# Kernel optimization log

Hardware: AMD Instinct MI355X
Metric: run time of the kernel (lower is better)

## Reference

```python
import jax, jax.numpy as jnp
import numpy as np

N, E = 20000, 200000
DIM, EDGE_DIM, HID = 128, 64, 256


def _linear_init(key, fan_in, fan_out):
    # torch nn.Linear default: U(-1/sqrt(fan_in), 1/sqrt(fan_in)) for W and b
    kw, kb = jax.random.split(key)
    bound = 1.0 / np.sqrt(fan_in)
    W = jax.random.uniform(kw, (fan_in, fan_out), minval=-bound, maxval=bound, dtype=jnp.float32)
    b = jax.random.uniform(kb, (fan_out,), minval=-bound, maxval=bound, dtype=jnp.float32)
    return W, b


def setup_inputs() -> dict:
    key = jax.random.key(0)
    ks = jax.random.split(key, 8)
    H = jax.random.normal(ks[0], (N, DIM), dtype=jnp.float32)
    src = jax.random.randint(ks[1], (E,), 0, N, dtype=jnp.int32)
    dst = jax.random.randint(ks[2], (E,), 0, N, dtype=jnp.int32)
    edge_index = jnp.stack([src, dst], axis=0)
    edge_attr = jax.random.normal(ks[3], (E, EDGE_DIM), dtype=jnp.float32)
    msg_W1, msg_b1 = _linear_init(ks[4], DIM + EDGE_DIM, HID)
    msg_W2, msg_b2 = _linear_init(ks[5], HID, DIM)
    self_W1, self_b1 = _linear_init(ks[6], DIM, HID)
    self_W2, self_b2 = _linear_init(ks[7], HID, DIM)
    eps = jnp.zeros((1,), dtype=jnp.float32)
    return dict(H=H, edge_index=edge_index, edge_attr=edge_attr, eps=eps,
                msg_W1=msg_W1, msg_b1=msg_b1, msg_W2=msg_W2, msg_b2=msg_b2,
                self_W1=self_W1, self_b1=self_b1, self_W2=self_W2, self_b2=self_b2)


def _mlp(x, W1, b1, W2, b2):
    h = jax.nn.relu(x @ W1 + b1)
    return h @ W2 + b2


def reference(H, edge_index, edge_attr, eps,
              msg_W1, msg_b1, msg_W2, msg_b2,
              self_W1, self_b1, self_W2, self_b2):
    src, dst = edge_index[0], edge_index[1]
    # gather source node features, concat edge features -> per-edge message MLP
    msg_in = jnp.concatenate([H[src], edge_attr], axis=-1)  # [E, dim+edge_dim]
    msg = _mlp(msg_in, msg_W1, msg_b1, msg_W2, msg_b2)       # [E, dim]
    # scatter-add messages to destination nodes
    agg = jax.ops.segment_sum(msg, dst, num_segments=H.shape[0])  # [N, dim]
    return _mlp((1.0 + eps) * H + agg, self_W1, self_b1, self_W2, self_b2)
```

## Files before the change

kernel.cpp:

```cpp
#include <hip/hip_runtime.h>

typedef float  f32x4  __attribute__((ext_vector_type(4)));
typedef short  bf16x8 __attribute__((ext_vector_type(8)));
typedef unsigned short u16;

#define NN   20000
#define NE   200000
#define DIM  128
#define EDIM 64
#define HID  256
#define KIN  192

__device__ __forceinline__ u16 f2b(float f) {
  unsigned u = __float_as_uint(f);
  u += 0x7FFFu + ((u >> 16) & 1u);
  return (u16)(u >> 16);
}
__device__ __forceinline__ float b2f(u16 v) {
  return __uint_as_float(((unsigned)v) << 16);
}

__global__ void prep_kernel(const float* __restrict__ mW1, const float* __restrict__ mW2,
                            const float* __restrict__ sW1, const float* __restrict__ sW2,
                            u16* __restrict__ W1T, u16* __restrict__ W2T,
                            u16* __restrict__ S1T, u16* __restrict__ S2T) {
  int t  = blockIdx.x * blockDim.x + threadIdx.x;
  int nt = gridDim.x * blockDim.x;
  for (int i = t; i < KIN * HID; i += nt) { int k = i / HID, n = i % HID; W1T[n * KIN + k] = f2b(mW1[i]); }
  for (int i = t; i < HID * DIM; i += nt) { int k = i / DIM, n = i % DIM; W2T[n * HID + k] = f2b(mW2[i]); }
  for (int i = t; i < DIM * HID; i += nt) { int k = i / HID, n = i % HID; S1T[n * DIM + k] = f2b(sW1[i]); }
  for (int i = t; i < HID * DIM; i += nt) { int k = i / DIM, n = i % DIM; S2T[n * HID + k] = f2b(sW2[i]); }
}

__global__ void hist_kernel(const int* __restrict__ EI, int* __restrict__ cnt) {
  int i = blockIdx.x * 256 + threadIdx.x;
  if (i < NE) atomicAdd(&cnt[EI[NE + i]], 1);
}

__global__ __launch_bounds__(1024) void scan_kernel(const int* __restrict__ cnt,
                                                    int* __restrict__ start,
                                                    int* __restrict__ cursor) {
  __shared__ int ls[1024];
  const int t = threadIdx.x;
  const int base = t * 20;
  int v[20]; int s = 0;
  #pragma unroll
  for (int j = 0; j < 20; ++j) {
    int idx = base + j;
    int c = (idx < NN) ? cnt[idx] : 0;
    v[j] = s; s += c;
  }
  ls[t] = s;
  __syncthreads();
  for (int off = 1; off < 1024; off <<= 1) {
    int x = (t >= off) ? ls[t - off] : 0;
    __syncthreads();
    ls[t] += x;
    __syncthreads();
  }
  int boff = (t > 0) ? ls[t - 1] : 0;
  #pragma unroll
  for (int j = 0; j < 20; ++j) {
    int idx = base + j;
    if (idx < NN) { int val = boff + v[j]; start[idx] = val; cursor[idx] = val; }
  }
  if (t == 0) start[NN] = NE;
}

__global__ __launch_bounds__(256, 4) void edge_kernel(
    const float* __restrict__ H, const int* __restrict__ EI,
    const float* __restrict__ EA,
    const u16* __restrict__ W1T, const float* __restrict__ b1p,
    const u16* __restrict__ W2T, const float* __restrict__ b2p,
    int* __restrict__ cursor, u16* __restrict__ msg) {
  __shared__ int src_s[64];
  __shared__ int pos_s[64];
  __shared__ u16 smem[64 * HID];

  const int tid = threadIdx.x;
  const int e0  = blockIdx.x * 64;
  if (tid < 64) {
    int e = e0 + tid;
    src_s[tid] = EI[e];
    pos_s[tid] = atomicAdd(&cursor[EI[NE + e]], 1);
  }
  __syncthreads();

  #pragma unroll
  for (int i = 0; i < 8; ++i) {
    int idx = tid + i * 256;
    int row = idx >> 5, c4 = idx & 31;
    const float4 v = reinterpret_cast<const float4*>(H + (size_t)src_s[row] * DIM)[c4];
    int by = (c4 * 8) ^ ((row & 7) << 4);
    ushort4 o; o.x = f2b(v.x); o.y = f2b(v.y); o.z = f2b(v.z); o.w = f2b(v.w);
    *reinterpret_cast<ushort4*>(&smem[row * KIN + (by >> 1)]) = o;
  }
  #pragma unroll
  for (int i = 0; i < 4; ++i) {
    int idx = tid + i * 256;
    int row = idx >> 4, c4 = idx & 15;
    const float4 v = reinterpret_cast<const float4*>(EA + (size_t)(e0 + row) * EDIM)[c4];
    int by = (256 + c4 * 8) ^ ((row & 7) << 4);
    ushort4 o; o.x = f2b(v.x); o.y = f2b(v.y); o.z = f2b(v.z); o.w = f2b(v.w);
    *reinterpret_cast<ushort4*>(&smem[row * KIN + (by >> 1)]) = o;
  }
  __syncthreads();

  const int wv = tid >> 6, lane = tid & 63;
  const int lr = lane & 15, lg = lane >> 4;
  const f32x4 zero = {0.f, 0.f, 0.f, 0.f};

  const int n0 = wv * 64;
  f32x4 acc[4][4];
  #pragma unroll
  for (int m = 0; m < 4; ++m)
    #pragma unroll
    for (int n = 0; n < 4; ++n) acc[m][n] = zero;
  float bias1[4];
  #pragma unroll
  for (int n = 0; n < 4; ++n) bias1[n] = b1p[n0 + n * 16 + lr];

  #pragma unroll
  for (int kt = 0; kt < 6; ++kt) {
    bf16x8 af[4], bf[4];
    #pragma unroll
    for (int m = 0; m < 4; ++m) {
      int row = m * 16 + lr;
      int by  = (kt * 64 + lg * 16) ^ ((row & 7) << 4);
      af[m] = *reinterpret_cast<const bf16x8*>(&smem[row * KIN + (by >> 1)]);
    }
    #pragma unroll
    for (int n = 0; n < 4; ++n) {
      int nabs = n0 + n * 16 + lr;
      bf[n] = *reinterpret_cast<const bf16x8*>(&W1T[nabs * KIN + kt * 32 + lg * 8]);
    }
    #pragma unroll
    for (int m = 0; m < 4; ++m)
      #pragma unroll
      for (int n = 0; n < 4; ++n)
        acc[m][n] = __builtin_amdgcn_mfma_f32_16x16x32_bf16(af[m], bf[n], acc[m][n], 0, 0, 0);
  }
  __syncthreads();

  #pragma unroll
  for (int m = 0; m < 4; ++m)
    #pragma unroll
    for (int n = 0; n < 4; ++n)
      #pragma unroll
      for (int r = 0; r < 4; ++r) {
        int row = m * 16 + lg * 4 + r;
        int col = n0 + n * 16 + lr;
        float v = acc[m][n][r] + bias1[n];
        v = fmaxf(v, 0.0f);
        int by = (col * 2) ^ ((row & 7) << 4);
        smem[row * HID + (by >> 1)] = f2b(v);
      }
  __syncthreads();

  const int n0b = wv * 32;
  f32x4 acc2[4][2];
  #pragma unroll
  for (int m = 0; m < 4; ++m) { acc2[m][0] = zero; acc2[m][1] = zero; }
  float bias2[2];
  #pragma unroll
  for (int n = 0; n < 2; ++n) bias2[n] = b2p[n0b + n * 16 + lr];

  #pragma unroll
  for (int kt = 0; kt < 8; ++kt) {
    bf16x8 af[4], bf[2];
    #pragma unroll
    for (int m = 0; m < 4; ++m) {
      int row = m * 16 + lr;
      int by  = (kt * 64 + lg * 16) ^ ((row & 7) << 4);
      af[m] = *reinterpret_cast<const bf16x8*>(&smem[row * HID + (by >> 1)]);
    }
    #pragma unroll
    for (int n = 0; n < 2; ++n) {
      int nabs = n0b + n * 16 + lr;
      bf[n] = *reinterpret_cast<const bf16x8*>(&W2T[nabs * HID + kt * 32 + lg * 8]);
    }
    #pragma unroll
    for (int m = 0; m < 4; ++m)
      #pragma unroll
      for (int n = 0; n < 2; ++n)
        acc2[m][n] = __builtin_amdgcn_mfma_f32_16x16x32_bf16(af[m], bf[n], acc2[m][n], 0, 0, 0);
  }

  #pragma unroll
  for (int m = 0; m < 4; ++m)
    #pragma unroll
    for (int n = 0; n < 2; ++n) {
      int col = n0b + n * 16 + lr;
      float bb = bias2[n];
      #pragma unroll
      for (int r = 0; r < 4; ++r) {
        int row = m * 16 + lg * 4 + r;
        msg[(size_t)pos_s[row] * DIM + col] = f2b(acc2[m][n][r] + bb);
      }
    }
}

__global__ __launch_bounds__(256, 6) void node_kernel(
    const float* __restrict__ H, const u16* __restrict__ msg,
    const int* __restrict__ start_g, const float* __restrict__ epsp,
    const u16* __restrict__ S1T, const float* __restrict__ b1p,
    const u16* __restrict__ S2T, const float* __restrict__ b2p,
    float* __restrict__ out) {
  __shared__ int start_s[33];
  __shared__ u16 smem[32 * HID];
  const int tid = threadIdx.x;
  const int r0  = blockIdx.x * 32;
  const float sc = 1.0f + epsp[0];

  if (tid < 33) start_s[tid] = start_g[r0 + tid];
  __syncthreads();

  {
    const int node = tid >> 3;
    const int c0   = (tid & 7) * 16;
    float a[16];
    #pragma unroll
    for (int j = 0; j < 16; ++j) a[j] = 0.f;
    const int s0 = start_s[node], s1 = start_s[node + 1];
    for (int i = s0; i < s1; ++i) {
      const u16* rp = msg + (size_t)i * DIM + c0;
      bf16x8 lo = *reinterpret_cast<const bf16x8*>(rp);
      bf16x8 hi = *reinterpret_cast<const bf16x8*>(rp + 8);
      #pragma unroll
      for (int j = 0; j < 8; ++j) {
        a[j]     += b2f((u16)lo[j]);
        a[8 + j] += b2f((u16)hi[j]);
      }
    }
    const int gr = r0 + node;
    const float4* hp = reinterpret_cast<const float4*>(H + (size_t)gr * DIM + c0);
    #pragma unroll
    for (int q = 0; q < 4; ++q) {
      float4 h = hp[q];
      ushort4 o;
      o.x = f2b(sc * h.x + a[q * 4 + 0]);
      o.y = f2b(sc * h.y + a[q * 4 + 1]);
      o.z = f2b(sc * h.z + a[q * 4 + 2]);
      o.w = f2b(sc * h.w + a[q * 4 + 3]);
      int col = c0 + q * 4;
      int by = (col * 2) ^ ((node & 7) << 4);
      *reinterpret_cast<ushort4*>(&smem[node * DIM + (by >> 1)]) = o;
    }
  }
  __syncthreads();

  const int wv = tid >> 6, lane = tid & 63;
  const int lr = lane & 15, lg = lane >> 4;
  const f32x4 zero = {0.f, 0.f, 0.f, 0.f};

  const int n0 = wv * 64;
  f32x4 acc[2][4];
  #pragma unroll
  for (int m = 0; m < 2; ++m)
    #pragma unroll
    for (int n = 0; n < 4; ++n) acc[m][n] = zero;
  float bias1[4];
  #pragma unroll
  for (int n = 0; n < 4; ++n) bias1[n] = b1p[n0 + n * 16 + lr];

  #pragma unroll
  for (int kt = 0; kt < 4; ++kt) {
    bf16x8 af[2], bf[4];
    #pragma unroll
    for (int m = 0; m < 2; ++m) {
      int row = m * 16 + lr;
      int by  = (kt * 64 + lg * 16) ^ ((row & 7) << 4);
      af[m] = *reinterpret_cast<const bf16x8*>(&smem[row * DIM + (by >> 1)]);
    }
    #pragma unroll
    for (int n = 0; n < 4; ++n) {
      int nabs = n0 + n * 16 + lr;
      bf[n] = *reinterpret_cast<const bf16x8*>(&S1T[nabs * DIM + kt * 32 + lg * 8]);
    }
    #pragma unroll
    for (int m = 0; m < 2; ++m)
      #pragma unroll
      for (int n = 0; n < 4; ++n)
        acc[m][n] = __builtin_amdgcn_mfma_f32_16x16x32_bf16(af[m], bf[n], acc[m][n], 0, 0, 0);
  }
  __syncthreads();

  #pragma unroll
  for (int m = 0; m < 2; ++m)
    #pragma unroll
    for (int n = 0; n < 4; ++n)
      #pragma unroll
      for (int r = 0; r < 4; ++r) {
        int row = m * 16 + lg * 4 + r;
        int col = n0 + n * 16 + lr;
        float v = acc[m][n][r] + bias1[n];
        v = fmaxf(v, 0.0f);
        int by = (col * 2) ^ ((row & 7) << 4);
        smem[row * HID + (by >> 1)] = f2b(v);
      }
  __syncthreads();

  const int n0b = wv * 32;
  f32x4 acc2[2][2];
  #pragma unroll
  for (int m = 0; m < 2; ++m) { acc2[m][0] = zero; acc2[m][1] = zero; }
  float bias2[2];
  #pragma unroll
  for (int n = 0; n < 2; ++n) bias2[n] = b2p[n0b + n * 16 + lr];

  #pragma unroll
  for (int kt = 0; kt < 8; ++kt) {
    bf16x8 af[2], bf[2];
    #pragma unroll
    for (int m = 0; m < 2; ++m) {
      int row = m * 16 + lr;
      int by  = (kt * 64 + lg * 16) ^ ((row & 7) << 4);
      af[m] = *reinterpret_cast<const bf16x8*>(&smem[row * HID + (by >> 1)]);
    }
    #pragma unroll
    for (int n = 0; n < 2; ++n) {
      int nabs = n0b + n * 16 + lr;
      bf[n] = *reinterpret_cast<const bf16x8*>(&S2T[nabs * HID + kt * 32 + lg * 8]);
    }
    #pragma unroll
    for (int m = 0; m < 2; ++m)
      #pragma unroll
      for (int n = 0; n < 2; ++n)
        acc2[m][n] = __builtin_amdgcn_mfma_f32_16x16x32_bf16(af[m], bf[n], acc2[m][n], 0, 0, 0);
  }

  #pragma unroll
  for (int m = 0; m < 2; ++m)
    #pragma unroll
    for (int n = 0; n < 2; ++n) {
      int col = n0b + n * 16 + lr;
      float bb = bias2[n];
      #pragma unroll
      for (int r = 0; r < 4; ++r) {
        int row = m * 16 + lg * 4 + r;
        int gr  = r0 + row;
        out[(size_t)gr * DIM + col] = acc2[m][n][r] + bb;
      }
    }
}

extern "C" void kernel_launch(void* const* d_in, const int* in_sizes, int n_in,
                              void* d_out, int out_size, void* d_ws, size_t ws_size,
                              hipStream_t stream) {
  const float* H   = (const float*)d_in[0];
  const int*   EI  = (const int*)  d_in[1];
  const float* EA  = (const float*)d_in[2];
  const float* EPS = (const float*)d_in[3];
  const float* mW1 = (const float*)d_in[4];
  const float* mb1 = (const float*)d_in[5];
  const float* mW2 = (const float*)d_in[6];
  const float* mb2 = (const float*)d_in[7];
  const float* sW1 = (const float*)d_in[8];
  const float* sb1 = (const float*)d_in[9];
  const float* sW2 = (const float*)d_in[10];
  const float* sb2 = (const float*)d_in[11];
  float* out = (float*)d_out;

  char* ws = (char*)d_ws;
  size_t off = 0;
  int* cnt    = (int*)(ws + off); off += (size_t)NN * 4;
  int* start  = (int*)(ws + off); off += (size_t)(NN + 1) * 4;
  int* cursor = (int*)(ws + off); off += (size_t)NN * 4;
  u16* W1T = (u16*)(ws + off); off += (size_t)HID * KIN * 2;
  u16* W2T = (u16*)(ws + off); off += (size_t)DIM * HID * 2;
  u16* S1T = (u16*)(ws + off); off += (size_t)HID * DIM * 2;
  u16* S2T = (u16*)(ws + off); off += (size_t)DIM * HID * 2;
  off = (off + 511) & ~(size_t)511;
  u16* msg = (u16*)(ws + off); off += (size_t)NE * DIM * 2;

  hipMemsetAsync(cnt, 0, (size_t)NN * 4, stream);
  prep_kernel<<<96, 256, 0, stream>>>(mW1, mW2, sW1, sW2, W1T, W2T, S1T, S2T);
  hist_kernel<<<(NE + 255) / 256, 256, 0, stream>>>(EI, cnt);
  scan_kernel<<<1, 1024, 0, stream>>>(cnt, start, cursor);
  edge_kernel<<<NE / 64, 256, 0, stream>>>(H, EI, EA, W1T, mb1, W2T, mb2, cursor, msg);
  node_kernel<<<NN / 32, 256, 0, stream>>>(H, msg, start, EPS, S1T, sb1, S2T, sb2, out);
}
```

Before: 253.4 us.

## Fuse scatter-add into edge kernel via dst-sorted edges and segmented reduction

Edges are first sorted by destination in a separate scatter pass that writes a permutation plus source and destination arrays. The edge kernel then processes edges in dst-sorted order and reduces each block's messages per destination segment in shared memory. Interior segments are stored directly and boundary segments are added with float atomics into an fp32 agg buffer. This removes the bf16 message buffer (E x 128) round-trip and the node-side gather loop. In exchange it adds a 10 MB memset, an extra scatter kernel, and an edge_attr gather by permutation; a serial 64-row reduction done by only 128 threads; and nondeterministic atomic summation.

```diff
diff --git a/kernel.cpp b/kernel.cpp
--- a/kernel.cpp
+++ b/kernel.cpp
@@ -15,9 +15,6 @@
   unsigned u = __float_as_uint(f);
   u += 0x7FFFu + ((u >> 16) & 1u);
   return (u16)(u >> 16);
-}
-__device__ __forceinline__ float b2f(u16 v) {
-  return __uint_as_float(((unsigned)v) << 16);
 }
 
 __global__ void prep_kernel(const float* __restrict__ mW1, const float* __restrict__ mW2,
@@ -38,7 +35,6 @@
 }
 
 __global__ __launch_bounds__(1024) void scan_kernel(const int* __restrict__ cnt,
-                                                    int* __restrict__ start,
                                                     int* __restrict__ cursor) {
   __shared__ int ls[1024];
   const int t = threadIdx.x;
@@ -62,27 +58,41 @@
   #pragma unroll
   for (int j = 0; j < 20; ++j) {
     int idx = base + j;
-    if (idx < NN) { int val = boff + v[j]; start[idx] = val; cursor[idx] = val; }
-  }
-  if (t == 0) start[NN] = NE;
+    if (idx < NN) cursor[idx] = boff + v[j];
+  }
+}
+
+__global__ void scatter_kernel(const int* __restrict__ EI, int* __restrict__ cursor,
+                               int* __restrict__ perm, int* __restrict__ srcs,
+                               int* __restrict__ dsts) {
+  int i = blockIdx.x * 256 + threadIdx.x;
+  if (i < NE) {
+    int d = EI[NE + i];
+    int pos = atomicAdd(&cursor[d], 1);
+    perm[pos] = i;
+    srcs[pos] = EI[i];
+    dsts[pos] = d;
+  }
 }
 
 __global__ __launch_bounds__(256, 4) void edge_kernel(
-    const float* __restrict__ H, const int* __restrict__ EI,
-    const float* __restrict__ EA,
+    const float* __restrict__ H, const float* __restrict__ EA,
+    const int* __restrict__ perm, const int* __restrict__ srcs,
+    const int* __restrict__ dsts,
     const u16* __restrict__ W1T, const float* __restrict__ b1p,
     const u16* __restrict__ W2T, const float* __restrict__ b2p,
-    int* __restrict__ cursor, u16* __restrict__ msg) {
+    float* __restrict__ agg) {
   __shared__ int src_s[64];
-  __shared__ int pos_s[64];
+  __shared__ int eid_s[64];
+  __shared__ int dst_s[64];
   __shared__ u16 smem[64 * HID];
 
   const int tid = threadIdx.x;
   const int e0  = blockIdx.x * 64;
   if (tid < 64) {
-    int e = e0 + tid;
-    src_s[tid] = EI[e];
-    pos_s[tid] = atomicAdd(&cursor[EI[NE + e]], 1);
+    src_s[tid] = srcs[e0 + tid];
+    eid_s[tid] = perm[e0 + tid];
+    dst_s[tid] = dsts[e0 + tid];
   }
   __syncthreads();
 
@@ -99,7 +109,7 @@
   for (int i = 0; i < 4; ++i) {
     int idx = tid + i * 256;
     int row = idx >> 4, c4 = idx & 15;
-    const float4 v = reinterpret_cast<const float4*>(EA + (size_t)(e0 + row) * EDIM)[c4];
+    const float4 v = reinterpret_cast<const float4*>(EA + (size_t)eid_s[row] * EDIM)[c4];
     int by = (256 + c4 * 8) ^ ((row & 7) << 4);
     ushort4 o; o.x = f2b(v.x); o.y = f2b(v.y); o.z = f2b(v.z); o.w = f2b(v.w);
     *reinterpret_cast<ushort4*>(&smem[row * KIN + (by >> 1)]) = o;
@@ -185,67 +195,64 @@
       for (int n = 0; n < 2; ++n)
         acc2[m][n] = __builtin_amdgcn_mfma_f32_16x16x32_bf16(af[m], bf[n], acc2[m][n], 0, 0, 0);
   }
-
+  __syncthreads();
+
+  float* msgf = reinterpret_cast<float*>(smem);
   #pragma unroll
   for (int m = 0; m < 4; ++m)
     #pragma unroll
     for (int n = 0; n < 2; ++n) {
+      float bb = bias2[n];
       int col = n0b + n * 16 + lr;
-      float bb = bias2[n];
       #pragma unroll
       for (int r = 0; r < 4; ++r) {
         int row = m * 16 + lg * 4 + r;
-        msg[(size_t)pos_s[row] * DIM + col] = f2b(acc2[m][n][r] + bb);
-      }
-    }
-}
-
-__global__ __launch_bounds__(256, 6) void node_kernel(
-    const float* __restrict__ H, const u16* __restrict__ msg,
-    const int* __restrict__ start_g, const float* __restrict__ epsp,
+        msgf[row * DIM + (col ^ ((row & 7) << 2))] = acc2[m][n][r] + bb;
+      }
+    }
+  __syncthreads();
+
+  if (tid < DIM) {
+    const int c = tid;
+    float s = 0.f;
+    int cur = dst_s[0];
+    int seg0 = 0;
+    for (int r = 0; r < 64; ++r) {
+      int d = dst_s[r];
+      if (d != cur) {
+        if (seg0 == 0) atomicAdd(&agg[(size_t)cur * DIM + c], s);
+        else           agg[(size_t)cur * DIM + c] = s;
+        s = 0.f; cur = d; seg0 = r;
+      }
+      s += msgf[r * DIM + (c ^ ((r & 7) << 2))];
+    }
+    atomicAdd(&agg[(size_t)cur * DIM + c], s);
+  }
+}
+
+__global__ __launch_bounds__(256, 6) void self_kernel(
+    const float* __restrict__ H, const float* __restrict__ agg,
+    const float* __restrict__ epsp,
     const u16* __restrict__ S1T, const float* __restrict__ b1p,
     const u16* __restrict__ S2T, const float* __restrict__ b2p,
     float* __restrict__ out) {
-  __shared__ int start_s[33];
   __shared__ u16 smem[32 * HID];
   const int tid = threadIdx.x;
   const int r0  = blockIdx.x * 32;
   const float sc = 1.0f + epsp[0];
 
-  if (tid < 33) start_s[tid] = start_g[r0 + tid];
-  __syncthreads();
-
-  {
-    const int node = tid >> 3;
-    const int c0   = (tid & 7) * 16;
-    float a[16];
-    #pragma unroll
-    for (int j = 0; j < 16; ++j) a[j] = 0.f;
-    const int s0 = start_s[node], s1 = start_s[node + 1];
-    for (int i = s0; i < s1; ++i) {
-      const u16* rp = msg + (size_t)i * DIM + c0;
-      bf16x8 lo = *reinterpret_cast<const bf16x8*>(rp);
-      bf16x8 hi = *reinterpret_cast<const bf16x8*>(rp + 8);
-      #pragma unroll
-      for (int j = 0; j < 8; ++j) {
-        a[j]     += b2f((u16)lo[j]);
-        a[8 + j] += b2f((u16)hi[j]);
-      }
-    }
-    const int gr = r0 + node;
-    const float4* hp = reinterpret_cast<const float4*>(H + (size_t)gr * DIM + c0);
-    #pragma unroll
-    for (int q = 0; q < 4; ++q) {
-      float4 h = hp[q];
-      ushort4 o;
-      o.x = f2b(sc * h.x + a[q * 4 + 0]);
-      o.y = f2b(sc * h.y + a[q * 4 + 1]);
-      o.z = f2b(sc * h.z + a[q * 4 + 2]);
-      o.w = f2b(sc * h.w + a[q * 4 + 3]);
-      int col = c0 + q * 4;
-      int by = (col * 2) ^ ((node & 7) << 4);
-      *reinterpret_cast<ushort4*>(&smem[node * DIM + (by >> 1)]) = o;
-    }
+  #pragma unroll
+  for (int i = 0; i < 4; ++i) {
+    int idx = tid + i * 256;
+    int row = idx >> 5, c4 = idx & 31;
+    int gr = r0 + row;
+    const float4 h = reinterpret_cast<const float4*>(H   + (size_t)gr * DIM)[c4];
+    const float4 a = reinterpret_cast<const float4*>(agg + (size_t)gr * DIM)[c4];
+    ushort4 o;
+    o.x = f2b(sc * h.x + a.x); o.y = f2b(sc * h.y + a.y);
+    o.z = f2b(sc * h.z + a.z); o.w = f2b(sc * h.w + a.w);
+    int by = (c4 * 8) ^ ((row & 7) << 4);
+    *reinterpret_cast<ushort4*>(&smem[row * DIM + (by >> 1)]) = o;
   }
   __syncthreads();
 
@@ -363,20 +370,24 @@
 
   char* ws = (char*)d_ws;
   size_t off = 0;
+  float* agg  = (float*)(ws + off); off += (size_t)NN * DIM * 4;
   int* cnt    = (int*)(ws + off); off += (size_t)NN * 4;
-  int* start  = (int*)(ws + off); off += (size_t)(NN + 1) * 4;
   int* cursor = (int*)(ws + off); off += (size_t)NN * 4;
+  int* perm   = (int*)(ws + off); off += (size_t)NE * 4;
+  int* srcs   = (int*)(ws + off); off += (size_t)NE * 4;
+  int* dsts   = (int*)(ws + off); off += (size_t)NE * 4;
   u16* W1T = (u16*)(ws + off); off += (size_t)HID * KIN * 2;
   u16* W2T = (u16*)(ws + off); off += (size_t)DIM * HID * 2;
   u16* S1T = (u16*)(ws + off); off += (size_t)HID * DIM * 2;
   u16* S2T = (u16*)(ws + off); off += (size_t)DIM * HID * 2;
-  off = (off + 511) & ~(size_t)511;
-  u16* msg = (u16*)(ws + off); off += (size_t)NE * DIM * 2;
-
+
+  hipMemsetAsync(agg, 0, (size_t)NN * DIM * 4, stream);
   hipMemsetAsync(cnt, 0, (size_t)NN * 4, stream);
   prep_kernel<<<96, 256, 0, stream>>>(mW1, mW2, sW1, sW2, W1T, W2T, S1T, S2T);
   hist_kernel<<<(NE + 255) / 256, 256, 0, stream>>>(EI, cnt);
-  scan_kernel<<<1, 1024, 0, stream>>>(cnt, start, cursor);
-  edge_kernel<<<NE / 64, 256, 0, stream>>>(H, EI, EA, W1T, mb1, W2T, mb2, cursor, msg);
-  node_kernel<<<NN / 32, 256, 0, stream>>>(H, msg, start, EPS, S1T, sb1, S2T, sb2, out);
-}
+  scan_kernel<<<1, 1024, 0, stream>>>(cnt, cursor);
+  scatter_kernel<<<(NE + 255) / 256, 256, 0, stream>>>(EI, cursor, perm, srcs, dsts);
+  edge_kernel<<<NE / 64, 256, 0, stream>>>(H, EA, perm, srcs, dsts,
+                                           W1T, mb1, W2T, mb2, agg);
+  self_kernel<<<NN / 32, 256, 0, stream>>>(H, agg, EPS, S1T, sb1, S2T, sb2, out);
+}
```

After: 256.9 us. No clear change (+1.4%).
